# Optimization experiments

Hardware: AMD Instinct MI355X
Metric: run time of the kernel (lower is better)

## Reference

```python
import jax, jax.numpy as jnp
import numpy as np

# Module hyperparameters (from init_kwargs)
K = 1.0                       # init_curvature (registered buffer, non-trainable)
HOPFIELD_DIM = 64
BETA = 1.0 / np.sqrt(float(HOPFIELD_DIM))  # beta=None default -> 1/sqrt(d_h)
EPS = 1e-7

# ---- Lorentz / hyperboloid ops (geoopt conventions, curvature param k>0) ----

def _to_tangent0(x):
    # x: (..., d) Euclidean -> (..., d+1) in T_0 H via [0, x], norm-clipped to 3.5
    zeros = jnp.zeros(x.shape[:-1] + (1,), x.dtype)
    x = jnp.concatenate([zeros, x], axis=-1)
    n = jnp.linalg.norm(x, axis=-1, keepdims=True)
    factor = jnp.minimum(3.5 / (n + 1e-7), 1.0)
    return x * factor

def expmap0(x_euc):
    # (..., d) Euclidean -> (..., d+1) on hyperboloid via Exp_0([0, x])
    u = _to_tangent0(x_euc)
    x = u[..., 1:]
    sqrtk = jnp.sqrt(K)
    xn = jnp.maximum(jnp.linalg.norm(x, axis=-1, keepdims=True), EPS)
    theta = xn / sqrtk
    return jnp.concatenate(
        [sqrtk * jnp.cosh(theta), sqrtk * jnp.sinh(theta) * x / xn], axis=-1)

def logmap0(y):
    # (..., d+1) on hyperboloid -> (..., d) tangent at origin (spatial part)
    sqrtk = jnp.sqrt(K)
    y0 = y[..., :1]
    yr = y[..., 1:]
    yn = jnp.maximum(jnp.linalg.norm(yr, axis=-1, keepdims=True), EPS)
    d = sqrtk * jnp.arccosh(jnp.maximum(y0 / sqrtk, 1.0 + EPS))
    return d * yr / yn

def minkowski_inner(u, v):
    # <u,v>_L = -u0 v0 + sum_i u_i v_i ; returns (...) without last dim
    return -u[..., 0] * v[..., 0] + jnp.sum(u[..., 1:] * v[..., 1:], axis=-1)

# ---- KFCore forward ----

def _kfcore(queries, keys, values, Wq, bq, Wk, bk, Wv, bv):
    sqrtk = jnp.sqrt(K)
    Qe = queries @ Wq.T + bq                     # (B,S,d_h)
    Ke = keys @ Wk.T + bk                        # (B,M,d_h)
    Ve = (values @ Wk.T + bk) @ Wv.T + bv        # (B,M,d_out)
    Q = expmap0(Qe)                              # (B,S,d+1)
    Kh = expmap0(Ke)                             # (B,M,d+1)
    V = expmap0(Ve)                              # (B,M,d+1)

    dp1 = Q.shape[-1]
    sign = jnp.concatenate([-jnp.ones((1,), Q.dtype), jnp.ones((dp1 - 1,), Q.dtype)])

    # Minkowski inner pairwise: (B,S,M)
    sims = jnp.einsum('bsd,bmd->bsm', Q * sign, Kh)
    alpha = jax.nn.softmax(-BETA * sims, axis=-1)          # (B,S,M)

    # Karcher flow: tangent_mean = sum_m alpha * logmap_Q(V_m)
    # logmap_x(y) = dist(x,y) * (y + (<x,y>/k) x) / ||y + (<x,y>/k) x||_L
    ip = jnp.einsum('bsd,bmd->bsm', Q * sign, V)           # <Q_s, V_m>_L
    dist = sqrtk * jnp.arccosh(jnp.maximum(-ip / K, 1.0 + EPS))
    qq = minkowski_inner(Q, Q)[:, :, None]                 # (B,S,1)
    vv = minkowski_inner(V, V)[:, None, :]                 # (B,1,M)
    c = ip / K
    nomin_sq = vv + 2.0 * c * ip + c * c * qq              # ||nomin||_L^2, (B,S,M)
    denom = jnp.sqrt(jnp.maximum(nomin_sq, EPS))
    w = alpha * dist / denom                               # (B,S,M)
    # sum_m w * (V_m + c * Q_s)  -- avoids the (B,S,M,d+1) logmap tensor
    tm = jnp.einsum('bsm,bmd->bsd', w, V) \
         + jnp.sum(w * c, axis=-1, keepdims=True) * Q      # (B,S,d+1)

    # expmap_Q(tm) = cosh(||tm||/sqrtk) Q + sqrtk sinh(||tm||/sqrtk) tm/||tm||
    un = jnp.sqrt(jnp.maximum(minkowski_inner(tm, tm), EPS))[..., None]
    th = un / sqrtk
    z = jnp.cosh(th) * Q + sqrtk * jnp.sinh(th) * tm / un
    return logmap0(z)                                      # (B,S,d_out)


def setup_inputs() -> dict:
    key = jax.random.key(0)
    ks = jax.random.split(key, 9)
    B, S, M = 2, 2048, 4096
    SD, MD, DH, DO = 256, 256, 64, 64
    sq = 1.0 / np.sqrt(SD)
    sm = 1.0 / np.sqrt(MD)
    sh = 1.0 / np.sqrt(DH)
    return {
        'queries': jax.random.normal(ks[0], (B, S, SD), jnp.float32),
        'keys':    jax.random.normal(ks[1], (B, M, MD), jnp.float32),
        'values':  jax.random.normal(ks[2], (B, M, MD), jnp.float32),
        'Wq': jax.random.normal(ks[3], (DH, SD), jnp.float32) * sq,
        'bq': jax.random.normal(ks[4], (DH,), jnp.float32) * sq,
        'Wk': jax.random.normal(ks[5], (DH, MD), jnp.float32) * sm,
        'bk': jax.random.normal(ks[6], (DH,), jnp.float32) * sm,
        'Wv': jax.random.normal(ks[7], (DO, DH), jnp.float32) * sh,
        'bv': jax.random.normal(ks[8], (DO,), jnp.float32) * sh,
    }


def reference(queries, keys, values, Wq, bq, Wk, bk, Wv, bv):
    return _kfcore(queries, keys, values, Wq, bq, Wk, bk, Wv, bv)
```

## Files before the change

kernel.cpp:

```cpp
#include <hip/hip_runtime.h>
#include <math.h>

#define BETA  0.125f
#define SHIFT 30.0f
#define EPSF  1e-7f

typedef __attribute__((ext_vector_type(8))) short short8;
typedef __attribute__((ext_vector_type(4))) short short4v;
typedef __attribute__((ext_vector_type(4))) float f32x4;

__device__ __forceinline__ unsigned short bf16_rne(float x) {
  unsigned int u = __float_as_uint(x);
  return (unsigned short)((u + 0x7fffu + ((u >> 16) & 1u)) >> 16);
}
__device__ __forceinline__ float bf16_tof(unsigned short h) {
  return __uint_as_float(((unsigned int)h) << 16);
}
__device__ __forceinline__ void split2(float x, unsigned short& h, unsigned short& l) {
  unsigned int u = __float_as_uint(x);
  unsigned int hr = (u + 0x7fffu + ((u >> 16) & 1u)) & 0xffff0000u;
  h = (unsigned short)(hr >> 16);
  l = bf16_rne(x - __uint_as_float(hr));
}
__device__ __forceinline__ void store4(unsigned short* ph, unsigned short* pl, float4 v) {
  unsigned short h0, h1, h2, h3, l0, l1, l2, l3;
  split2(v.x, h0, l0); split2(v.y, h1, l1);
  split2(v.z, h2, l2); split2(v.w, h3, l3);
  *(uint2*)ph = make_uint2((unsigned)h0 | ((unsigned)h1 << 16),
                           (unsigned)h2 | ((unsigned)h3 << 16));
  *(uint2*)pl = make_uint2((unsigned)l0 | ((unsigned)l1 << 16),
                           (unsigned)l2 | ((unsigned)l3 << 16));
}

#define ZERO_F4 68608

__global__ __launch_bounds__(256) void proj_kernel(
    const float* __restrict__ Xq, const float* __restrict__ Xk,
    const float* __restrict__ Xv,
    const float* __restrict__ Wq, const float* __restrict__ bq,
    const float* __restrict__ Wk, const float* __restrict__ bk,
    const float* __restrict__ Wv, const float* __restrict__ bv,
    float* __restrict__ Q0, float* __restrict__ K0, float* __restrict__ V0,
    unsigned short* __restrict__ Qh, unsigned short* __restrict__ Ql,
    unsigned short* __restrict__ Kh, unsigned short* __restrict__ Kl,
    unsigned short* __restrict__ Vh, unsigned short* __restrict__ Vl,
    unsigned short* __restrict__ Vth, unsigned short* __restrict__ Vtl,
    float* __restrict__ zeroRegion)
{
  __shared__ unsigned short LB[18432];

  const int bid = blockIdx.x;
  const int tid = threadIdx.x;

  {
    int idx = bid * 256 + tid;
    if (idx < ZERO_F4)
      *(float4*)&zeroRegion[idx * 4] = make_float4(0.f, 0.f, 0.f, 0.f);
  }

  const float *X, *W, *bias;
  float* y0;
  unsigned short *yh, *yl;
  bool dbl;
  int rowBase;
  if (bid < 128)      { X = Xv; W = Wk; bias = bk; y0 = V0; yh = Vh; yl = Vl; rowBase = bid << 6;         dbl = true;  }
  else if (bid < 256) { X = Xk; W = Wk; bias = bk; y0 = K0; yh = Kh; yl = Kl; rowBase = (bid - 128) << 6; dbl = false; }
  else                { X = Xq; W = Wq; bias = bq; y0 = Q0; yh = Qh; yl = Ql; rowBase = (bid - 256) << 6; dbl = false; }

  const int wave = tid >> 6, lane = tid & 63;
  const int lm = lane & 15;
  const int lg = lane >> 4;
  const int rowB = rowBase + (wave << 4);

  f32x4 acc[4];
#pragma unroll
  for (int nj = 0; nj < 4; ++nj) {
    float b = bias[nj * 16 + lm];
    acc[nj] = f32x4{b, b, b, b};
  }

  for (int kc = 0; kc < 4; ++kc) {
#pragma unroll
    for (int q = 0; q < 4; ++q) {
      int f = tid + (q << 8);
      int r = f >> 4, g = f & 15;
      float4 xv = *(const float4*)&X[(rowBase + r) * 256 + (kc << 6) + (g << 2)];
      float4 wv = *(const float4*)&W[r * 256 + (kc << 6) + (g << 2)];
      int o = r * 72 + (g << 2);
      store4(&LB[o],         &LB[4608 + o],  xv);
      store4(&LB[9216 + o],  &LB[13824 + o], wv);
    }
    __syncthreads();
    short8 Ah2[2], Al2[2];
#pragma unroll
    for (int ks = 0; ks < 2; ++ks) {
      int ao = (wave * 16 + lm) * 72 + ks * 32 + lg * 8;
      Ah2[ks] = *(const short8*)&LB[ao];
      Al2[ks] = *(const short8*)&LB[4608 + ao];
    }
#pragma unroll
    for (int nj = 0; nj < 4; ++nj) {
#pragma unroll
      for (int ks = 0; ks < 2; ++ks) {
        int bo = (nj * 16 + lm) * 72 + ks * 32 + lg * 8;
        short8 Bh = *(const short8*)&LB[9216 + bo];
        short8 Bl = *(const short8*)&LB[13824 + bo];
        acc[nj] = __builtin_amdgcn_mfma_f32_16x16x32_bf16(Ah2[ks], Bh, acc[nj], 0, 0, 0);
        acc[nj] = __builtin_amdgcn_mfma_f32_16x16x32_bf16(Ah2[ks], Bl, acc[nj], 0, 0, 0);
        acc[nj] = __builtin_amdgcn_mfma_f32_16x16x32_bf16(Al2[ks], Bh, acc[nj], 0, 0, 0);
      }
    }
    __syncthreads();
  }

  if (dbl) {
#pragma unroll
    for (int nj = 0; nj < 4; ++nj)
#pragma unroll
      for (int r = 0; r < 4; ++r) {
        unsigned short h, l;
        split2(acc[nj][r], h, l);
        int ro = (wave * 16 + lg * 4 + r) * 72 + nj * 16 + lm;
        LB[ro] = h;
        LB[4608 + ro] = l;
      }
#pragma unroll
    for (int q = 0; q < 4; ++q) {
      int f = tid + (q << 8);
      int r = f >> 4, g = f & 15;
      float4 wv = *(const float4*)&Wv[r * 64 + (g << 2)];
      int o = r * 72 + (g << 2);
      store4(&LB[9216 + o], &LB[13824 + o], wv);
    }
    __syncthreads();
    short8 A2h[2], A2l[2];
#pragma unroll
    for (int ks = 0; ks < 2; ++ks) {
      int ao = (wave * 16 + lm) * 72 + ks * 32 + lg * 8;
      A2h[ks] = *(const short8*)&LB[ao];
      A2l[ks] = *(const short8*)&LB[4608 + ao];
    }
#pragma unroll
    for (int nj = 0; nj < 4; ++nj) {
      float b = bv[nj * 16 + lm];
      acc[nj] = f32x4{b, b, b, b};
    }
#pragma unroll
    for (int nj = 0; nj < 4; ++nj) {
#pragma unroll
      for (int ks = 0; ks < 2; ++ks) {
        int bo = (nj * 16 + lm) * 72 + ks * 32 + lg * 8;
        short8 Bh = *(const short8*)&LB[9216 + bo];
        short8 Bl = *(const short8*)&LB[13824 + bo];
        acc[nj] = __builtin_amdgcn_mfma_f32_16x16x32_bf16(A2h[ks], Bh, acc[nj], 0, 0, 0);
        acc[nj] = __builtin_amdgcn_mfma_f32_16x16x32_bf16(A2h[ks], Bl, acc[nj], 0, 0, 0);
        acc[nj] = __builtin_amdgcn_mfma_f32_16x16x32_bf16(A2l[ks], Bh, acc[nj], 0, 0, 0);
      }
    }
  }

  float n2p[4];
#pragma unroll
  for (int r = 0; r < 4; ++r)
    n2p[r] = acc[0][r] * acc[0][r] + acc[1][r] * acc[1][r] +
             acc[2][r] * acc[2][r] + acc[3][r] * acc[3][r];
#pragma unroll
  for (int r = 0; r < 4; ++r) {
    n2p[r] += __shfl_xor(n2p[r], 1);
    n2p[r] += __shfl_xor(n2p[r], 2);
    n2p[r] += __shfl_xor(n2p[r], 4);
    n2p[r] += __shfl_xor(n2p[r], 8);
  }
  unsigned short hv[4][4], lv[4][4];
#pragma unroll
  for (int r = 0; r < 4; ++r) {
    float n = sqrtf(n2p[r]);
    float factor = fminf(3.5f / (n + EPSF), 1.0f);
    float xn = fmaxf(n * factor, EPSF);
    float et = __expf(xn);
    float rt = __builtin_amdgcn_rcpf(et);
    float ch = 0.5f * (et + rt);
    float sh = 0.5f * (et - rt);
    float scale = sh * factor * __builtin_amdgcn_rcpf(xn);
    int row = rowB + lg * 4 + r;
    if (lm == 0) y0[row] = ch;
#pragma unroll
    for (int nj = 0; nj < 4; ++nj) {
      split2(acc[nj][r] * scale, hv[r][nj], lv[r][nj]);
      yh[row * 64 + nj * 16 + lm] = hv[r][nj];
      yl[row * 64 + nj * 16 + lm] = lv[r][nj];
    }
  }

  if (dbl) {
    __syncthreads();
    unsigned int* Tr = (unsigned int*)LB;
#pragma unroll
    for (int r = 0; r < 4; ++r)
#pragma unroll
      for (int nj = 0; nj < 4; ++nj)
        Tr[(wave * 16 + lg * 4 + r) * 65 + nj * 16 + lm] = (unsigned int)hv[r][nj];
    __syncthreads();
#pragma unroll
    for (int q = 0; q < 2; ++q) {
      int f = tid + (q << 8);
      int d = f >> 3;
      int seg = (f & 7) << 3;
      unsigned int o[4];
#pragma unroll
      for (int k = 0; k < 4; ++k)
        o[k] = Tr[(seg + 2 * k) * 65 + d] | (Tr[(seg + 2 * k + 1) * 65 + d] << 16);
      *(uint4*)&Vth[d * 8192 + rowBase + seg] = make_uint4(o[0], o[1], o[2], o[3]);
    }
    __syncthreads();
#pragma unroll
    for (int r = 0; r < 4; ++r)
#pragma unroll
      for (int nj = 0; nj < 4; ++nj)
        Tr[(wave * 16 + lg * 4 + r) * 65 + nj * 16 + lm] = (unsigned int)lv[r][nj];
    __syncthreads();
#pragma unroll
    for (int q = 0; q < 2; ++q) {
      int f = tid + (q << 8);
      int d = f >> 3;
      int seg = (f & 7) << 3;
      unsigned int o[4];
#pragma unroll
      for (int k = 0; k < 4; ++k)
        o[k] = Tr[(seg + 2 * k) * 65 + d] | (Tr[(seg + 2 * k + 1) * 65 + d] << 16);
      *(uint4*)&Vtl[d * 8192 + rowBase + seg] = make_uint4(o[0], o[1], o[2], o[3]);
    }
  }
}

__global__ void __attribute__((amdgpu_waves_per_eu(4)))
__launch_bounds__(256) attn_kernel(
    const float* __restrict__ Q0g, const unsigned short* __restrict__ Qh,
    const unsigned short* __restrict__ Ql,
    const float* __restrict__ K0g, const unsigned short* __restrict__ Khg,
    const unsigned short* __restrict__ Klg,
    const float* __restrict__ V0g, const unsigned short* __restrict__ Vhg,
    const unsigned short* __restrict__ Vlg,
    const unsigned short* __restrict__ Vthg, const unsigned short* __restrict__ Vtlg,
    float* __restrict__ Tacc, float* __restrict__ T0acc,
    float* __restrict__ Lacc, float* __restrict__ WCacc)
{
  __shared__ unsigned short LB[16640];

  const int tid = threadIdx.x;
  const int wave = tid >> 6, lane = tid & 63;
  const int lm = lane & 15;
  const int lg = lane >> 4;
  const int bid = blockIdx.x;
  const int slice = bid & 15;
  const int t = bid >> 4;
  const int b = t >> 5;
  const int sT = t & 31;
  const int sBase = b * 2048 + sT * 64 + wave * 16;

  unsigned short* wbase = LB + 14336 + wave * 576;

  short8 qf[2][2];
#pragma unroll
  for (int ks = 0; ks < 2; ++ks) {
    int idx = (sBase + lm) * 64 + ks * 32 + lg * 8;
    qf[ks][0] = *(const short8*)(Qh + idx);
    qf[ks][1] = *(const short8*)(Ql + idx);
  }
  float q0r[4];
#pragma unroll
  for (int r = 0; r < 4; ++r) q0r[r] = Q0g[sBase + lg * 4 + r];

  f32x4 accT[4];
  float Lp[4], WCp[4], T0p[4];
#pragma unroll
  for (int r = 0; r < 4; ++r) { Lp[r] = 0.f; WCp[r] = 0.f; T0p[r] = 0.f; }
#pragma unroll
  for (int dj = 0; dj < 4; ++dj) accT[dj] = f32x4{0.f, 0.f, 0.f, 0.f};

  const int mSliceBase = b * 4096 + slice * 256;
  const int srow = tid >> 3;
  const int sc8 = (tid & 7) << 3;
  const int drow = tid >> 2;
  const int dseg = (tid & 3) << 3;

  for (int mc = 0; mc < 8; ++mc) {
    const int mCh = mSliceBase + (mc << 5);

    {
      int goff = (mCh + srow) * 64 + sc8;
      int loff = srow * 72 + sc8;
      *(uint4*)&LB[loff]         = *(const uint4*)&Khg[goff];
      *(uint4*)&LB[2304 + loff]  = *(const uint4*)&Klg[goff];
      *(uint4*)&LB[4608 + loff]  = *(const uint4*)&Vhg[goff];
      *(uint4*)&LB[6912 + loff]  = *(const uint4*)&Vlg[goff];
      int gofft = drow * 8192 + mCh + dseg;
      int lofft = drow * 40 + dseg;
      *(uint4*)&LB[9216 + lofft]  = *(const uint4*)&Vthg[gofft];
      *(uint4*)&LB[11776 + lofft] = *(const uint4*)&Vtlg[gofft];
    }
    float k0r[2], v0r[2];
#pragma unroll
    for (int mj = 0; mj < 2; ++mj) {
      k0r[mj] = K0g[mCh + mj * 16 + lm];
      v0r[mj] = V0g[mCh + mj * 16 + lm];
    }
    __syncthreads();

#pragma unroll
    for (int mj = 0; mj < 2; ++mj) {
      f32x4 sims = f32x4{0.f, 0.f, 0.f, 0.f};
      f32x4 ipv  = f32x4{0.f, 0.f, 0.f, 0.f};
#pragma unroll
      for (int ks = 0; ks < 2; ++ks) {
        int off = (mj * 16 + lm) * 72 + ks * 32 + lg * 8;
        short8 kh = *(const short8*)&LB[off];
        short8 kl = *(const short8*)&LB[2304 + off];
        short8 vh = *(const short8*)&LB[4608 + off];
        short8 vl = *(const short8*)&LB[6912 + off];
        sims = __builtin_amdgcn_mfma_f32_16x16x32_bf16(qf[ks][0], kh, sims, 0, 0, 0);
        sims = __builtin_amdgcn_mfma_f32_16x16x32_bf16(qf[ks][0], kl, sims, 0, 0, 0);
        sims = __builtin_amdgcn_mfma_f32_16x16x32_bf16(qf[ks][1], kh, sims, 0, 0, 0);
        ipv  = __builtin_amdgcn_mfma_f32_16x16x32_bf16(qf[ks][0], vh, ipv, 0, 0, 0);
        ipv  = __builtin_amdgcn_mfma_f32_16x16x32_bf16(qf[ks][0], vl, ipv, 0, 0, 0);
        ipv  = __builtin_amdgcn_mfma_f32_16x16x32_bf16(qf[ks][1], vh, ipv, 0, 0, 0);
      }
#pragma unroll
      for (int r = 0; r < 4; ++r) {
        float c  = ipv[r]  - q0r[r] * v0r[mj];
        float sm = sims[r] - q0r[r] * k0r[mj];
        float x = -c;
        float s2 = fmaxf(fmaf(x, x, -1.0f), EPSF);
        float rs = __builtin_amdgcn_rsqf(s2);
        float dist = __logf(fmaf(s2, rs, x));
        float e = __expf(fmaf(-BETA, sm, -SHIFT));
        float w = e * dist * rs;
        unsigned short wu = bf16_rne(w);
        float wb = bf16_tof(wu);
        Lp[r]  += e;
        WCp[r] += wb * c;
        T0p[r] += wb * v0r[mj];
        wbase[(lg * 4 + r) * 36 + mj * 16 + lm] = wu;
      }
    }

    {
      short8 wa;
      {
        const unsigned short* p = wbase + lm * 36 + lg * 8;
        short4v a0 = *(const short4v*)p;
        short4v a1 = *(const short4v*)(p + 4);
        wa = __builtin_shufflevector(a0, a1, 0, 1, 2, 3, 4, 5, 6, 7);
      }
#pragma unroll
      for (int dj = 0; dj < 4; ++dj) {
        int off = (dj * 16 + lm) * 40 + lg * 8;
        short8 th = *(const short8*)&LB[9216 + off];
        short8 tl = *(const short8*)&LB[11776 + off];
        accT[dj] = __builtin_amdgcn_mfma_f32_16x16x32_bf16(wa, th, accT[dj], 0, 0, 0);
        accT[dj] = __builtin_amdgcn_mfma_f32_16x16x32_bf16(wa, tl, accT[dj], 0, 0, 0);
      }
    }
    __syncthreads();
  }

#pragma unroll
  for (int r = 0; r < 4; ++r)
#pragma unroll
    for (int off = 1; off < 16; off <<= 1) {
      Lp[r]  += __shfl_xor(Lp[r], off);
      WCp[r] += __shfl_xor(WCp[r], off);
      T0p[r] += __shfl_xor(T0p[r], off);
    }

#pragma unroll
  for (int r = 0; r < 4; ++r) {
    int row = sBase + lg * 4 + r;
#pragma unroll
    for (int dj = 0; dj < 4; ++dj)
      unsafeAtomicAdd(&Tacc[row * 64 + dj * 16 + lm], accT[dj][r]);
    if (lm == 0) {
      unsafeAtomicAdd(&Lacc[row],  Lp[r]);
      unsafeAtomicAdd(&WCacc[row], WCp[r]);
      unsafeAtomicAdd(&T0acc[row], T0p[r]);
    }
  }
}

__global__ __launch_bounds__(256) void combine_kernel(
    const float* __restrict__ Q0, const unsigned short* __restrict__ Qh,
    const unsigned short* __restrict__ Ql,
    const float* __restrict__ Tacc, const float* __restrict__ T0acc,
    const float* __restrict__ Lacc, const float* __restrict__ WCacc,
    float* __restrict__ out)
{
  int wid = (blockIdx.x << 2) + (threadIdx.x >> 6);
  int lane = threadIdx.x & 63;

  int qi = wid * 64 + lane;
  float Tsum = Tacc[qi];
  float T0 = T0acc[wid];
  float L  = Lacc[wid];
  float WC = WCacc[wid];

  float qd = bf16_tof(Qh[qi]) + bf16_tof(Ql[qi]);
  float q0 = Q0[wid];
  float invL = 1.0f / L;
  float td = Tsum * invL;
  float t0 = T0 * invL;
  float wc = WC * invL;

  double tt = (double)td * (double)td;
#pragma unroll
  for (int off = 1; off < 64; off <<= 1) tt += __shfl_xor(tt, off);
  tt -= (double)t0 * (double)t0;
  double mk = tt + (double)wc * (double)wc;

  float un = (float)sqrt(fmax(mk, 1e-12));
  float eu = __expf(un);
  float ru = 1.0f / eu;
  float ch = 0.5f * (eu + ru);
  float shu = 0.5f * (eu - ru) / un;

  float tmd = td + wc * qd;
  float tm0 = t0 + wc * q0;
  float zd = ch * qd + shu * tmd;
  float z0 = ch * q0 + shu * tm0;

  float p2 = zd * zd;
#pragma unroll
  for (int off = 1; off < 64; off <<= 1) p2 += __shfl_xor(p2, off);
  float yn = fmaxf(sqrtf(p2), EPSF);
  float zc = fmaxf(z0, 1.0f + EPSF);
  float dl = __logf(zc + sqrtf(fmaxf(zc * zc - 1.0f, 0.f)));
  out[qi] = dl * zd / yn;
}

extern "C" void kernel_launch(void* const* d_in, const int* in_sizes, int n_in,
                              void* d_out, int out_size, void* d_ws, size_t ws_size,
                              hipStream_t stream)
{
  const float* queries = (const float*)d_in[0];
  const float* keys    = (const float*)d_in[1];
  const float* values  = (const float*)d_in[2];
  const float* Wq      = (const float*)d_in[3];
  const float* bq      = (const float*)d_in[4];
  const float* Wk      = (const float*)d_in[5];
  const float* bk      = (const float*)d_in[6];
  const float* Wv      = (const float*)d_in[7];
  const float* bv      = (const float*)d_in[8];
  float* out = (float*)d_out;
  float* ws  = (float*)d_ws;

  float* Q0 = ws;
  float* K0 = ws + 4096;
  float* V0 = ws + 12288;
  unsigned short* Qh  = (unsigned short*)(ws + 20480);
  unsigned short* Ql  = (unsigned short*)(ws + 151552);
  unsigned short* Kh  = (unsigned short*)(ws + 282624);
  unsigned short* Kl  = (unsigned short*)(ws + 544768);
  unsigned short* Vh  = (unsigned short*)(ws + 806912);
  unsigned short* Vl  = (unsigned short*)(ws + 1069056);
  unsigned short* Vth = (unsigned short*)(ws + 1331200);
  unsigned short* Vtl = (unsigned short*)(ws + 1593344);
  float* Tacc  = ws + 1855488;
  float* T0acc = ws + 2117632;
  float* Lacc  = ws + 2121728;
  float* WCacc = ws + 2125824;

  proj_kernel<<<320, 256, 0, stream>>>(queries, keys, values, Wq, bq, Wk, bk,
                                       Wv, bv, Q0, K0, V0, Qh, Ql, Kh, Kl,
                                       Vh, Vl, Vth, Vtl, Tacc);
  attn_kernel<<<1024, 256, 0, stream>>>(
      Q0, Qh, Ql, K0, Kh, Kl, V0, Vh, Vl, Vth, Vtl,
      Tacc, T0acc, Lacc, WCacc);
  combine_kernel<<<1024, 256, 0, stream>>>(
      Q0, Qh, Ql, Tacc, T0acc, Lacc, WCacc, out);
}
```

Before: 135.2 us.

## Split projection tiles to 32 rows and divide columns across waves

The projection kernel now handles 32 rows per block instead of 64, doubling the grid to 640 blocks. Each wave computes a 16x32 output quadrant, and row norms are combined across the two column-half waves through shared memory. The V transpose is rewritten to match. This is meant to fill more of the GPU's compute units in the proj stage, at the cost of reloading the weight tile twice as often and adding an extra barrier.

```diff
diff --git a/kernel.cpp b/kernel.cpp
--- a/kernel.cpp
+++ b/kernel.cpp
@@ -47,7 +47,8 @@
     unsigned short* __restrict__ Vth, unsigned short* __restrict__ Vtl,
     float* __restrict__ zeroRegion)
 {
-  __shared__ unsigned short LB[18432];
+  __shared__ unsigned short LB[13824];
+  __shared__ float npart[2][2][16];
 
   const int bid = blockIdx.x;
   const int tid = threadIdx.x;
@@ -63,51 +64,58 @@
   unsigned short *yh, *yl;
   bool dbl;
   int rowBase;
-  if (bid < 128)      { X = Xv; W = Wk; bias = bk; y0 = V0; yh = Vh; yl = Vl; rowBase = bid << 6;         dbl = true;  }
-  else if (bid < 256) { X = Xk; W = Wk; bias = bk; y0 = K0; yh = Kh; yl = Kl; rowBase = (bid - 128) << 6; dbl = false; }
-  else                { X = Xq; W = Wq; bias = bq; y0 = Q0; yh = Qh; yl = Ql; rowBase = (bid - 256) << 6; dbl = false; }
+  if (bid < 256)      { X = Xv; W = Wk; bias = bk; y0 = V0; yh = Vh; yl = Vl; rowBase = bid << 5;         dbl = true;  }
+  else if (bid < 512) { X = Xk; W = Wk; bias = bk; y0 = K0; yh = Kh; yl = Kl; rowBase = (bid - 256) << 5; dbl = false; }
+  else                { X = Xq; W = Wq; bias = bq; y0 = Q0; yh = Qh; yl = Ql; rowBase = (bid - 512) << 5; dbl = false; }
 
   const int wave = tid >> 6, lane = tid & 63;
   const int lm = lane & 15;
   const int lg = lane >> 4;
-  const int rowB = rowBase + (wave << 4);
-
-  f32x4 acc[4];
-#pragma unroll
-  for (int nj = 0; nj < 4; ++nj) {
-    float b = bias[nj * 16 + lm];
-    acc[nj] = f32x4{b, b, b, b};
+  const int rg = wave & 1;
+  const int colBase = (wave >> 1) << 5;
+
+  f32x4 acc[2];
+#pragma unroll
+  for (int njh = 0; njh < 2; ++njh) {
+    float b = bias[colBase + njh * 16 + lm];
+    acc[njh] = f32x4{b, b, b, b};
   }
 
   for (int kc = 0; kc < 4; ++kc) {
+#pragma unroll
+    for (int q = 0; q < 2; ++q) {
+      int f = tid + (q << 8);
+      int r = f >> 4, g = f & 15;
+      float4 xv = *(const float4*)&X[(rowBase + r) * 256 + (kc << 6) + (g << 2)];
+      int o = r * 72 + (g << 2);
+      store4(&LB[o], &LB[2304 + o], xv);
+    }
 #pragma unroll
     for (int q = 0; q < 4; ++q) {
       int f = tid + (q << 8);
       int r = f >> 4, g = f & 15;
-      float4 xv = *(const float4*)&X[(rowBase + r) * 256 + (kc << 6) + (g << 2)];
       float4 wv = *(const float4*)&W[r * 256 + (kc << 6) + (g << 2)];
       int o = r * 72 + (g << 2);
-      store4(&LB[o],         &LB[4608 + o],  xv);
-      store4(&LB[9216 + o],  &LB[13824 + o], wv);
+      store4(&LB[4608 + o], &LB[9216 + o], wv);
     }
     __syncthreads();
     short8 Ah2[2], Al2[2];
 #pragma unroll
     for (int ks = 0; ks < 2; ++ks) {
-      int ao = (wave * 16 + lm) * 72 + ks * 32 + lg * 8;
+      int ao = (rg * 16 + lm) * 72 + ks * 32 + lg * 8;
       Ah2[ks] = *(const short8*)&LB[ao];
-      Al2[ks] = *(const short8*)&LB[4608 + ao];
-    }
-#pragma unroll
-    for (int nj = 0; nj < 4; ++nj) {
+      Al2[ks] = *(const short8*)&LB[2304 + ao];
+    }
+#pragma unroll
+    for (int njh = 0; njh < 2; ++njh) {
 #pragma unroll
       for (int ks = 0; ks < 2; ++ks) {
-        int bo = (nj * 16 + lm) * 72 + ks * 32 + lg * 8;
-        short8 Bh = *(const short8*)&LB[9216 + bo];
-        short8 Bl = *(const short8*)&LB[13824 + bo];
-        acc[nj] = __builtin_amdgcn_mfma_f32_16x16x32_bf16(Ah2[ks], Bh, acc[nj], 0, 0, 0);
-        acc[nj] = __builtin_amdgcn_mfma_f32_16x16x32_bf16(Ah2[ks], Bl, acc[nj], 0, 0, 0);
-        acc[nj] = __builtin_amdgcn_mfma_f32_16x16x32_bf16(Al2[ks], Bh, acc[nj], 0, 0, 0);
+        int bo = (colBase + njh * 16 + lm) * 72 + ks * 32 + lg * 8;
+        short8 Bh = *(const short8*)&LB[4608 + bo];
+        short8 Bl = *(const short8*)&LB[9216 + bo];
+        acc[njh] = __builtin_amdgcn_mfma_f32_16x16x32_bf16(Ah2[ks], Bh, acc[njh], 0, 0, 0);
+        acc[njh] = __builtin_amdgcn_mfma_f32_16x16x32_bf16(Ah2[ks], Bl, acc[njh], 0, 0, 0);
+        acc[njh] = __builtin_amdgcn_mfma_f32_16x16x32_bf16(Al2[ks], Bh, acc[njh], 0, 0, 0);
       }
     }
     __syncthreads();
@@ -115,14 +123,14 @@
 
   if (dbl) {
 #pragma unroll
-    for (int nj = 0; nj < 4; ++nj)
+    for (int njh = 0; njh < 2; ++njh)
 #pragma unroll
       for (int r = 0; r < 4; ++r) {
         unsigned short h, l;
-        split2(acc[nj][r], h, l);
-        int ro = (wave * 16 + lg * 4 + r) * 72 + nj * 16 + lm;
+        split2(acc[njh][r], h, l);
+        int ro = (rg * 16 + lg * 4 + r) * 72 + colBase + njh * 16 + lm;
         LB[ro] = h;
-        LB[4608 + ro] = l;
+        LB[2304 + ro] = l;
       }
 #pragma unroll
     for (int q = 0; q < 4; ++q) {
@@ -130,31 +138,31 @@
       int r = f >> 4, g = f & 15;
       float4 wv = *(const float4*)&Wv[r * 64 + (g << 2)];
       int o = r * 72 + (g << 2);
-      store4(&LB[9216 + o], &LB[13824 + o], wv);
+      store4(&LB[4608 + o], &LB[9216 + o], wv);
     }
     __syncthreads();
     short8 A2h[2], A2l[2];
 #pragma unroll
     for (int ks = 0; ks < 2; ++ks) {
-      int ao = (wave * 16 + lm) * 72 + ks * 32 + lg * 8;
+      int ao = (rg * 16 + lm) * 72 + ks * 32 + lg * 8;
       A2h[ks] = *(const short8*)&LB[ao];
-      A2l[ks] = *(const short8*)&LB[4608 + ao];
-    }
-#pragma unroll
-    for (int nj = 0; nj < 4; ++nj) {
-      float b = bv[nj * 16 + lm];
-      acc[nj] = f32x4{b, b, b, b};
-    }
-#pragma unroll
-    for (int nj = 0; nj < 4; ++nj) {
+      A2l[ks] = *(const short8*)&LB[2304 + ao];
+    }
+#pragma unroll
+    for (int njh = 0; njh < 2; ++njh) {
+      float b = bv[colBase + njh * 16 + lm];
+      acc[njh] = f32x4{b, b, b, b};
+    }
+#pragma unroll
+    for (int njh = 0; njh < 2; ++njh) {
 #pragma unroll
       for (int ks = 0; ks < 2; ++ks) {
-        int bo = (nj * 16 + lm) * 72 + ks * 32 + lg * 8;
-        short8 Bh = *(const short8*)&LB[9216 + bo];
-        short8 Bl = *(const short8*)&LB[13824 + bo];
-        acc[nj] = __builtin_amdgcn_mfma_f32_16x16x32_bf16(A2h[ks], Bh, acc[nj], 0, 0, 0);
-        acc[nj] = __builtin_amdgcn_mfma_f32_16x16x32_bf16(A2h[ks], Bl, acc[nj], 0, 0, 0);
-        acc[nj] = __builtin_amdgcn_mfma_f32_16x16x32_bf16(A2l[ks], Bh, acc[nj], 0, 0, 0);
+        int bo = (colBase + njh * 16 + lm) * 72 + ks * 32 + lg * 8;
+        short8 Bh = *(const short8*)&LB[4608 + bo];
+        short8 Bl = *(const short8*)&LB[9216 + bo];
+        acc[njh] = __builtin_amdgcn_mfma_f32_16x16x32_bf16(A2h[ks], Bh, acc[njh], 0, 0, 0);
+        acc[njh] = __builtin_amdgcn_mfma_f32_16x16x32_bf16(A2h[ks], Bl, acc[njh], 0, 0, 0);
+        acc[njh] = __builtin_amdgcn_mfma_f32_16x16x32_bf16(A2l[ks], Bh, acc[njh], 0, 0, 0);
       }
     }
   }
@@ -162,8 +170,7 @@
   float n2p[4];
 #pragma unroll
   for (int r = 0; r < 4; ++r)
-    n2p[r] = acc[0][r] * acc[0][r] + acc[1][r] * acc[1][r] +
-             acc[2][r] * acc[2][r] + acc[3][r] * acc[3][r];
+    n2p[r] = acc[0][r] * acc[0][r] + acc[1][r] * acc[1][r];
 #pragma unroll
   for (int r = 0; r < 4; ++r) {
     n2p[r] += __shfl_xor(n2p[r], 1);
@@ -171,10 +178,18 @@
     n2p[r] += __shfl_xor(n2p[r], 4);
     n2p[r] += __shfl_xor(n2p[r], 8);
   }
-  unsigned short hv[4][4], lv[4][4];
+  if (lm == 0) {
+#pragma unroll
+    for (int r = 0; r < 4; ++r)
+      npart[rg][wave >> 1][lg * 4 + r] = n2p[r];
+  }
+  __syncthreads();
+
+  unsigned short hv[4][2], lv[4][2];
 #pragma unroll
   for (int r = 0; r < 4; ++r) {
-    float n = sqrtf(n2p[r]);
+    float n2 = npart[rg][0][lg * 4 + r] + npart[rg][1][lg * 4 + r];
+    float n = sqrtf(n2);
     float factor = fminf(3.5f / (n + EPSF), 1.0f);
     float xn = fmaxf(n * factor, EPSF);
     float et = __expf(xn);
@@ -182,30 +197,27 @@
     float ch = 0.5f * (et + rt);
     float sh = 0.5f * (et - rt);
     float scale = sh * factor * __builtin_amdgcn_rcpf(xn);
-    int row = rowB + lg * 4 + r;
-    if (lm == 0) y0[row] = ch;
-#pragma unroll
-    for (int nj = 0; nj < 4; ++nj) {
-      split2(acc[nj][r] * scale, hv[r][nj], lv[r][nj]);
-      yh[row * 64 + nj * 16 + lm] = hv[r][nj];
-      yl[row * 64 + nj * 16 + lm] = lv[r][nj];
+    int row = rowBase + rg * 16 + lg * 4 + r;
+    if (lm == 0 && colBase == 0) y0[row] = ch;
+#pragma unroll
+    for (int njh = 0; njh < 2; ++njh) {
+      split2(acc[njh][r] * scale, hv[r][njh], lv[r][njh]);
+      yh[row * 64 + colBase + njh * 16 + lm] = hv[r][njh];
+      yl[row * 64 + colBase + njh * 16 + lm] = lv[r][njh];
     }
   }
 
   if (dbl) {
-    __syncthreads();
     unsigned int* Tr = (unsigned int*)LB;
 #pragma unroll
     for (int r = 0; r < 4; ++r)
 #pragma unroll
-      for (int nj = 0; nj < 4; ++nj)
-        Tr[(wave * 16 + lg * 4 + r) * 65 + nj * 16 + lm] = (unsigned int)hv[r][nj];
-    __syncthreads();
-#pragma unroll
-    for (int q = 0; q < 2; ++q) {
-      int f = tid + (q << 8);
-      int d = f >> 3;
-      int seg = (f & 7) << 3;
+      for (int njh = 0; njh < 2; ++njh)
+        Tr[(rg * 16 + lg * 4 + r) * 65 + colBase + njh * 16 + lm] = (unsigned int)hv[r][njh];
+    __syncthreads();
+    {
+      int d = tid >> 2;
+      int seg = (tid & 3) << 3;
       unsigned int o[4];
 #pragma unroll
       for (int k = 0; k < 4; ++k)
@@ -216,14 +228,12 @@
 #pragma unroll
     for (int r = 0; r < 4; ++r)
 #pragma unroll
-      for (int nj = 0; nj < 4; ++nj)
-        Tr[(wave * 16 + lg * 4 + r) * 65 + nj * 16 + lm] = (unsigned int)lv[r][nj];
-    __syncthreads();
-#pragma unroll
-    for (int q = 0; q < 2; ++q) {
-      int f = tid + (q << 8);
-      int d = f >> 3;
-      int seg = (f & 7) << 3;
+      for (int njh = 0; njh < 2; ++njh)
+        Tr[(rg * 16 + lg * 4 + r) * 65 + colBase + njh * 16 + lm] = (unsigned int)lv[r][njh];
+    __syncthreads();
+    {
+      int d = tid >> 2;
+      int seg = (tid & 3) << 3;
       unsigned int o[4];
 #pragma unroll
       for (int k = 0; k < 4; ++k)
@@ -468,7 +478,7 @@
   float* Lacc  = ws + 2121728;
   float* WCacc = ws + 2125824;
 
-  proj_kernel<<<320, 256, 0, stream>>>(queries, keys, values, Wq, bq, Wk, bk,
+  proj_kernel<<<640, 256, 0, stream>>>(queries, keys, values, Wq, bq, Wk, bk,
                                        Wv, bv, Q0, K0, V0, Qh, Ql, Kh, Kl,
                                        Vh, Vl, Vth, Vtl, Tacc);
   attn_kernel<<<1024, 256, 0, stream>>>(
```

Result: no change. 136.7 us (+1.1%).

## Fuse combine step into attention kernel via last-block-done counter

Applied to the files above, without the earlier changes.

The attention kernel now increments a per-query-tile counter after its atomic accumulations. The last of the 16 slice blocks for a tile then performs the combine/logmap epilogue inline, so the separate combine kernel launch goes away. The intent is to remove one kernel launch and the trip through global memory between kernels. In exchange it adds a memset, threadfences and a serial tail in the last block of each tile. The fused path only runs if the workspace is large enough to hold the counters; otherwise it falls back to the old two-launch path.

```diff
diff --git a/kernel.cpp b/kernel.cpp
--- a/kernel.cpp
+++ b/kernel.cpp
@@ -70,7 +70,6 @@
   const int wave = tid >> 6, lane = tid & 63;
   const int lm = lane & 15;
   const int lg = lane >> 4;
-  const int rowB = rowBase + (wave << 4);
 
   f32x4 acc[4];
 #pragma unroll
@@ -159,6 +158,7 @@
     }
   }
 
+  const int rowB = rowBase + (wave << 4);
   float n2p[4];
 #pragma unroll
   for (int r = 0; r < 4; ++r)
@@ -243,9 +243,11 @@
     const unsigned short* __restrict__ Vlg,
     const unsigned short* __restrict__ Vthg, const unsigned short* __restrict__ Vtlg,
     float* __restrict__ Tacc, float* __restrict__ T0acc,
-    float* __restrict__ Lacc, float* __restrict__ WCacc)
+    float* __restrict__ Lacc, float* __restrict__ WCacc,
+    int* __restrict__ doneCnt, float* __restrict__ out)
 {
   __shared__ unsigned short LB[16640];
+  __shared__ int lastFlag;
 
   const int tid = threadIdx.x;
   const int wave = tid >> 6, lane = tid & 63;
@@ -385,6 +387,56 @@
       unsafeAtomicAdd(&T0acc[row], T0p[r]);
     }
   }
+
+  if (doneCnt == nullptr) return;
+
+  __threadfence();
+  if (tid == 0) lastFlag = atomicAdd(&doneCnt[t], 1);
+  __syncthreads();
+  if (lastFlag != 15) return;
+  __threadfence();
+
+  const int rowW = (t << 6) + (wave << 4);
+  for (int rr = 0; rr < 16; ++rr) {
+    int row = rowW + rr;
+    int qi = row * 64 + lane;
+    float Tsum = __hip_atomic_load(&Tacc[qi],   __ATOMIC_RELAXED, __HIP_MEMORY_SCOPE_AGENT);
+    float T0   = __hip_atomic_load(&T0acc[row], __ATOMIC_RELAXED, __HIP_MEMORY_SCOPE_AGENT);
+    float L    = __hip_atomic_load(&Lacc[row],  __ATOMIC_RELAXED, __HIP_MEMORY_SCOPE_AGENT);
+    float WC   = __hip_atomic_load(&WCacc[row], __ATOMIC_RELAXED, __HIP_MEMORY_SCOPE_AGENT);
+
+    float qd = bf16_tof(Qh[qi]) + bf16_tof(Ql[qi]);
+    float q0 = Q0g[row];
+    float invL = 1.0f / L;
+    float td = Tsum * invL;
+    float t0 = T0 * invL;
+    float wc = WC * invL;
+
+    double tt = (double)td * (double)td;
+#pragma unroll
+    for (int off = 1; off < 64; off <<= 1) tt += __shfl_xor(tt, off);
+    tt -= (double)t0 * (double)t0;
+    double mk = tt + (double)wc * (double)wc;
+
+    float un = (float)sqrt(fmax(mk, 1e-12));
+    float eu = __expf(un);
+    float ru = 1.0f / eu;
+    float ch = 0.5f * (eu + ru);
+    float shu = 0.5f * (eu - ru) / un;
+
+    float tmd = td + wc * qd;
+    float tm0 = t0 + wc * q0;
+    float zd = ch * qd + shu * tmd;
+    float z0 = ch * q0 + shu * tm0;
+
+    float p2 = zd * zd;
+#pragma unroll
+    for (int off = 1; off < 64; off <<= 1) p2 += __shfl_xor(p2, off);
+    float yn = fmaxf(sqrtf(p2), EPSF);
+    float zc = fmaxf(z0, 1.0f + EPSF);
+    float dl = __logf(zc + sqrtf(fmaxf(zc * zc - 1.0f, 0.f)));
+    out[qi] = dl * zd / yn;
+  }
 }
 
 __global__ __launch_bounds__(256) void combine_kernel(
@@ -468,12 +520,23 @@
   float* Lacc  = ws + 2121728;
   float* WCacc = ws + 2125824;
 
+  const size_t baseFloats = 2129920;
+  bool fused = ws_size >= baseFloats * sizeof(float) + 64 * sizeof(int);
+  int* doneCnt = fused ? (int*)(ws + baseFloats) : nullptr;
+
   proj_kernel<<<320, 256, 0, stream>>>(queries, keys, values, Wq, bq, Wk, bk,
                                        Wv, bv, Q0, K0, V0, Qh, Ql, Kh, Kl,
                                        Vh, Vl, Vth, Vtl, Tacc);
-  attn_kernel<<<1024, 256, 0, stream>>>(
-      Q0, Qh, Ql, K0, Kh, Kl, V0, Vh, Vl, Vth, Vtl,
-      Tacc, T0acc, Lacc, WCacc);
-  combine_kernel<<<1024, 256, 0, stream>>>(
-      Q0, Qh, Ql, Tacc, T0acc, Lacc, WCacc, out);
-}
+  if (fused) {
+    hipMemsetAsync(doneCnt, 0, 64 * sizeof(int), stream);
+    attn_kernel<<<1024, 256, 0, stream>>>(
+        Q0, Qh, Ql, K0, Kh, Kl, V0, Vh, Vl, Vth, Vtl,
+        Tacc, T0acc, Lacc, WCacc, doneCnt, out);
+  } else {
+    attn_kernel<<<1024, 256, 0, stream>>>(
+        Q0, Qh, Ql, K0, Kh, Kl, V0, Vh, Vl, Vth, Vtl,
+        Tacc, T0acc, Lacc, WCacc, nullptr, nullptr);
+    combine_kernel<<<1024, 256, 0, stream>>>(
+        Q0, Qh, Ql, Tacc, T0acc, Lacc, WCacc, out);
+  }
+}
```

Measured after the change: 229.1 us. 69.4% more time.
